# Optimization experiments

Hardware: AMD Instinct MI355X
Metric: run time of the kernel (lower is better)

Reference implementation:

```python
import jax, jax.numpy as jnp
import numpy as np

N_GRID = 16      # reservoir_n
CHANNELS = 4
R = 2            # receptive-field radius -> 5x5 kernel
T_STEPS = 8
NEG_SLOPE = 0.1


def _extract_patches(S):
    # S: [b, C, n, n] -> patches [b, C, 5, 5, n, n] (kernel offsets u,v)
    Sp = jnp.pad(S, ((0, 0), (0, 0), (R, R), (R, R)))
    k = 2 * R + 1
    rows = [jnp.stack([Sp[:, :, du:du + N_GRID, dv:dv + N_GRID] for dv in range(k)], axis=2)
            for du in range(k)]
    return jnp.stack(rows, axis=2)  # [b, C, k, k, n, n]


def _reservoir_step(S, W):
    # W: [n, n, C_out, C_in, k, k]; per-pixel unique weights (locally connected)
    patches = _extract_patches(S)                       # [b, c, u, v, y, x]
    out = jnp.einsum('bcuvyx,yxocuv->boyx', patches, W)  # [b, C, n, n]
    return jnp.where(out > 0, out, NEG_SLOPE * out)      # leaky_relu(0.1)


def setup_inputs() -> dict:
    key = jax.random.key(0)
    k1, k2 = jax.random.split(key)
    x = jax.random.normal(k1, (8192, 784), dtype=jnp.float32)
    # scale weights down so the T-step recurrence stays numerically tame
    W = jax.random.normal(k2, (N_GRID, N_GRID, CHANNELS, CHANNELS, 2 * R + 1, 2 * R + 1),
                          dtype=jnp.float32) * 0.05
    return {"x": x, "W": W}


def reference(x, W):
    batch = x.shape[0]
    total = N_GRID * N_GRID * CHANNELS  # 1024
    padded = jnp.pad(x, ((0, 0), (0, total - x.shape[1])))
    S = padded.reshape(batch, CHANNELS, N_GRID, N_GRID)
    for _ in range(T_STEPS):
        S = _reservoir_step(S, W)
    S_pooled = S.mean(axis=1)                 # pool over channels -> [b, n, n]
    return S_pooled.reshape(batch, -1)        # [b, n*n]
```

## Files before the change

kernel.cpp:

```cpp
#include <hip/hip_runtime.h>

#define NG 16
#define NC 4
#define BPB 16
#define TSTEPS 8
#define PITCH 64
#define CROW (NG * PITCH)

__device__ __forceinline__ void fma4(float w, const float4& s, float4& a) {
    a.x = fmaf(w, s.x, a.x);
    a.y = fmaf(w, s.y, a.y);
    a.z = fmaf(w, s.z, a.z);
    a.w = fmaf(w, s.w, a.w);
}

__device__ __forceinline__ float4 lrelu4(float4 v) {
    float4 r;
    r.x = fmaxf(v.x, 0.1f * v.x);
    r.y = fmaxf(v.y, 0.1f * v.y);
    r.z = fmaxf(v.z, 0.1f * v.z);
    r.w = fmaxf(v.w, 0.1f * v.w);
    return r;
}

template<int CTRL>
__device__ __forceinline__ float dppf(float x) {
    return __int_as_float(__builtin_amdgcn_update_dpp(
        0, __float_as_int(x), CTRL, 0xF, 0xF, true));
}
template<int CTRL>
__device__ __forceinline__ float4 dpp4(float4 v) {
    float4 r;
    r.x = dppf<CTRL>(v.x);
    r.y = dppf<CTRL>(v.y);
    r.z = dppf<CTRL>(v.z);
    r.w = dppf<CTRL>(v.w);
    return r;
}

__global__ void wt_transpose(const float* __restrict__ W, float4* __restrict__ Wt) {
    int t = blockIdx.x * 256 + threadIdx.x;
    if (t >= 25600) return;
    int r = t >> 8;
    int pix = t & 255;
    int c = r / 25, uv = r - c * 25, u = uv / 5, v = uv - u * 5;
    int y = pix >> 4, x = pix & 15;
    float4 w = make_float4(0.f, 0.f, 0.f, 0.f);
    if ((unsigned)(y + u - 2) < 16u && (unsigned)(x + v - 2) < 16u) {
        int base = pix * 400 + c * 25 + uv;
        w.x = W[base];
        w.y = W[base + 100];
        w.z = W[base + 200];
        w.w = W[base + 300];
    }
    Wt[r * 256 + pix] = w;
}

__global__ __launch_bounds__(512, 2)
void reservoir_kernel(const float* __restrict__ X, const float4* __restrict__ Wt,
                      float* __restrict__ out, int batch) {
    __shared__ float4 smv[NC * CROW];
    float* smf = reinterpret_cast<float*>(smv);

    const int tid = threadIdx.x;
    const int oct = tid >> 8;
    const int pix = tid & 255;
    const int y = pix >> 4;
    const int x = pix & 15;
    const long itemBase = (long)blockIdx.x * BPB;

    const int sw = (x >> 1) & 3;
    const int xb = x << 2;
    const int q0 = (2 * oct) ^ sw;
    const int q1 = (2 * oct + 1) ^ sw;

    for (int b = 0; b < BPB; ++b) {
        long item = itemBase + b;
        #pragma unroll
        for (int k = 0; k < 2; ++k) {
            int idx = tid + k * 512;
            float v = 0.f;
            if (idx < 784 && item < batch)
                v = __builtin_nontemporal_load(&X[item * 784 + idx]);
            int c = idx >> 8, rem = idx & 255, yy = rem >> 4, xx = rem & 15;
            int phys = (b >> 2) ^ ((xx >> 1) & 3);
            smf[(((c * NG + yy) << 6) + (xx << 2) + phys) * 4 + (b & 3)] = v;
        }
    }

    const float4* Wp = Wt + pix;
    float4 w0 = Wp[0], w1 = Wp[256], w2 = Wp[512], w3 = Wp[768], w4 = Wp[1024];
    int wnext = 1280;

    __syncthreads();

#define TAP(WV, T0, T1) \
    fma4(WV.x, T0, a00); fma4(WV.x, T1, a01); \
    fma4(WV.y, T0, a10); fma4(WV.y, T1, a11); \
    fma4(WV.z, T0, a20); fma4(WV.z, T1, a21); \
    fma4(WV.w, T0, a30); fma4(WV.w, T1, a31);

    #pragma unroll 1
    for (int t = 0; t < TSTEPS; ++t) {
        float4 a00 = {0,0,0,0}, a01 = {0,0,0,0};
        float4 a10 = {0,0,0,0}, a11 = {0,0,0,0};
        float4 a20 = {0,0,0,0}, a21 = {0,0,0,0};
        float4 a30 = {0,0,0,0}, a31 = {0,0,0,0};

        #pragma unroll 1
        for (int c = 0; c < NC; ++c) {
            #pragma unroll 1
            for (int u = 0; u < 5; ++u) {
                int yy = y + u - 2;
                yy = yy < 0 ? 0 : (yy > 15 ? 15 : yy);
                const int rb = ((c * NG + yy) << 6) + xb;
                const float4 s0 = smv[rb + q0];
                const float4 s1 = smv[rb + q1];

                TAP(w2, s0, s1)
                w2 = Wp[wnext + 512];
                { const float4 t0 = dpp4<0x111>(s0), t1 = dpp4<0x111>(s1);
                  TAP(w1, t0, t1) }
                w1 = Wp[wnext + 256];
                { const float4 t0 = dpp4<0x101>(s0), t1 = dpp4<0x101>(s1);
                  TAP(w3, t0, t1) }
                w3 = Wp[wnext + 768];
                { const float4 t0 = dpp4<0x112>(s0), t1 = dpp4<0x112>(s1);
                  TAP(w0, t0, t1) }
                w0 = Wp[wnext];
                { const float4 t0 = dpp4<0x102>(s0), t1 = dpp4<0x102>(s1);
                  TAP(w4, t0, t1) }
                w4 = Wp[wnext + 1024];

                wnext += 1280;
                if (wnext >= 25600) wnext = 0;
            }
        }

        a00 = lrelu4(a00); a01 = lrelu4(a01);
        a10 = lrelu4(a10); a11 = lrelu4(a11);
        a20 = lrelu4(a20); a21 = lrelu4(a21);
        a30 = lrelu4(a30); a31 = lrelu4(a31);

        if (t < TSTEPS - 1) {
            __syncthreads();
            const int pb = (y << 6) + xb;
            smv[0 * CROW + pb + q0] = a00;  smv[0 * CROW + pb + q1] = a01;
            smv[1 * CROW + pb + q0] = a10;  smv[1 * CROW + pb + q1] = a11;
            smv[2 * CROW + pb + q0] = a20;  smv[2 * CROW + pb + q1] = a21;
            smv[3 * CROW + pb + q0] = a30;  smv[3 * CROW + pb + q1] = a31;
            __syncthreads();
        } else {
            float4 p0, p1;
            p0.x = (a00.x + a10.x + a20.x + a30.x) * 0.25f;
            p0.y = (a00.y + a10.y + a20.y + a30.y) * 0.25f;
            p0.z = (a00.z + a10.z + a20.z + a30.z) * 0.25f;
            p0.w = (a00.w + a10.w + a20.w + a30.w) * 0.25f;
            p1.x = (a01.x + a11.x + a21.x + a31.x) * 0.25f;
            p1.y = (a01.y + a11.y + a21.y + a31.y) * 0.25f;
            p1.z = (a01.z + a11.z + a21.z + a31.z) * 0.25f;
            p1.w = (a01.w + a11.w + a21.w + a31.w) * 0.25f;
            const long b0 = itemBase + 8 * oct;
            const long ob = b0 * 256 + pix;
            if (b0 + 0 < batch) __builtin_nontemporal_store(p0.x, &out[ob + 0 * 256]);
            if (b0 + 1 < batch) __builtin_nontemporal_store(p0.y, &out[ob + 1 * 256]);
            if (b0 + 2 < batch) __builtin_nontemporal_store(p0.z, &out[ob + 2 * 256]);
            if (b0 + 3 < batch) __builtin_nontemporal_store(p0.w, &out[ob + 3 * 256]);
            if (b0 + 4 < batch) __builtin_nontemporal_store(p1.x, &out[ob + 4 * 256]);
            if (b0 + 5 < batch) __builtin_nontemporal_store(p1.y, &out[ob + 5 * 256]);
            if (b0 + 6 < batch) __builtin_nontemporal_store(p1.z, &out[ob + 6 * 256]);
            if (b0 + 7 < batch) __builtin_nontemporal_store(p1.w, &out[ob + 7 * 256]);
        }
    }
}

extern "C" void kernel_launch(void* const* d_in, const int* in_sizes, int n_in,
                              void* d_out, int out_size, void* d_ws, size_t ws_size,
                              hipStream_t stream) {
    const float* X = (const float*)d_in[0];
    const float* W = (const float*)d_in[1];
    float* out = (float*)d_out;
    const int batch = in_sizes[0] / 784;
    const int blocks = (batch + BPB - 1) / BPB;

    wt_transpose<<<100, 256, 0, stream>>>(W, (float4*)d_ws);
    reservoir_kernel<<<blocks, 512, 0, stream>>>(
        X, (const float4*)d_ws, out, batch);
}
```

Measured before the change: 233.3 us.

## Halve block to 8 items and double-buffer state to drop one barrier per step

Each block now handles 8 batch items with 256 threads instead of 16 items with 512 threads. The reservoir state in shared memory is ping-ponged between two buffers, so the barrier before the write-back can be removed and only one __syncthreads per step remains. The shared-memory layout and swizzle are reworked for the new pitch. In exchange there are twice as many blocks, each loading the weight stream from global/L2 again, which doubles weight traffic per item, and the new swizzle may bring bank conflicts.

```diff
diff --git a/kernel.cpp b/kernel.cpp
--- a/kernel.cpp
+++ b/kernel.cpp
@@ -2,10 +2,8 @@
 
 #define NG 16
 #define NC 4
-#define BPB 16
+#define BPB 8
 #define TSTEPS 8
-#define PITCH 64
-#define CROW (NG * PITCH)
 
 __device__ __forceinline__ void fma4(float w, const float4& s, float4& a) {
     a.x = fmaf(w, s.x, a.x);
@@ -56,39 +54,36 @@
     Wt[r * 256 + pix] = w;
 }
 
-__global__ __launch_bounds__(512, 2)
+__global__ __launch_bounds__(256, 2)
 void reservoir_kernel(const float* __restrict__ X, const float4* __restrict__ Wt,
                       float* __restrict__ out, int batch) {
-    __shared__ float4 smv[NC * CROW];
+    __shared__ float4 smv[2 * NC * NG * NG * 2];
     float* smf = reinterpret_cast<float*>(smv);
 
     const int tid = threadIdx.x;
-    const int oct = tid >> 8;
-    const int pix = tid & 255;
-    const int y = pix >> 4;
-    const int x = pix & 15;
+    const int y = tid >> 4;
+    const int x = tid & 15;
     const long itemBase = (long)blockIdx.x * BPB;
 
-    const int sw = (x >> 1) & 3;
-    const int xb = x << 2;
-    const int q0 = (2 * oct) ^ sw;
-    const int q1 = (2 * oct + 1) ^ sw;
+    const int swx = (x >> 2) & 1;
+    const int q0 = swx;
+    const int q1 = swx ^ 1;
 
     for (int b = 0; b < BPB; ++b) {
         long item = itemBase + b;
         #pragma unroll
-        for (int k = 0; k < 2; ++k) {
-            int idx = tid + k * 512;
+        for (int k = 0; k < 4; ++k) {
+            int idx = tid + k * 256;
             float v = 0.f;
             if (idx < 784 && item < batch)
                 v = __builtin_nontemporal_load(&X[item * 784 + idx]);
             int c = idx >> 8, rem = idx & 255, yy = rem >> 4, xx = rem & 15;
-            int phys = (b >> 2) ^ ((xx >> 1) & 3);
-            smf[(((c * NG + yy) << 6) + (xx << 2) + phys) * 4 + (b & 3)] = v;
+            int phys = (b >> 2) ^ ((xx >> 2) & 1);
+            smf[((((c * NG + yy) * NG + xx) << 1) + phys) * 4 + (b & 3)] = v;
         }
     }
 
-    const float4* Wp = Wt + pix;
+    const float4* Wp = Wt + tid;
     float4 w0 = Wp[0], w1 = Wp[256], w2 = Wp[512], w3 = Wp[768], w4 = Wp[1024];
     int wnext = 1280;
 
@@ -102,6 +97,8 @@
 
     #pragma unroll 1
     for (int t = 0; t < TSTEPS; ++t) {
+        const int rbase = (t & 1) << 11;
+        const int wbase = rbase ^ 2048;
         float4 a00 = {0,0,0,0}, a01 = {0,0,0,0};
         float4 a10 = {0,0,0,0}, a11 = {0,0,0,0};
         float4 a20 = {0,0,0,0}, a21 = {0,0,0,0};
@@ -113,7 +110,7 @@
             for (int u = 0; u < 5; ++u) {
                 int yy = y + u - 2;
                 yy = yy < 0 ? 0 : (yy > 15 ? 15 : yy);
-                const int rb = ((c * NG + yy) << 6) + xb;
+                const int rb = rbase + (((c * NG + yy) * NG + x) << 1);
                 const float4 s0 = smv[rb + q0];
                 const float4 s1 = smv[rb + q1];
 
@@ -143,12 +140,11 @@
         a30 = lrelu4(a30); a31 = lrelu4(a31);
 
         if (t < TSTEPS - 1) {
-            __syncthreads();
-            const int pb = (y << 6) + xb;
-            smv[0 * CROW + pb + q0] = a00;  smv[0 * CROW + pb + q1] = a01;
-            smv[1 * CROW + pb + q0] = a10;  smv[1 * CROW + pb + q1] = a11;
-            smv[2 * CROW + pb + q0] = a20;  smv[2 * CROW + pb + q1] = a21;
-            smv[3 * CROW + pb + q0] = a30;  smv[3 * CROW + pb + q1] = a31;
+            const int pb = wbase + (((y * NG) + x) << 1);
+            smv[pb + 0 * 512 + q0] = a00;  smv[pb + 0 * 512 + q1] = a01;
+            smv[pb + 1 * 512 + q0] = a10;  smv[pb + 1 * 512 + q1] = a11;
+            smv[pb + 2 * 512 + q0] = a20;  smv[pb + 2 * 512 + q1] = a21;
+            smv[pb + 3 * 512 + q0] = a30;  smv[pb + 3 * 512 + q1] = a31;
             __syncthreads();
         } else {
             float4 p0, p1;
@@ -160,16 +156,15 @@
             p1.y = (a01.y + a11.y + a21.y + a31.y) * 0.25f;
             p1.z = (a01.z + a11.z + a21.z + a31.z) * 0.25f;
             p1.w = (a01.w + a11.w + a21.w + a31.w) * 0.25f;
-            const long b0 = itemBase + 8 * oct;
-            const long ob = b0 * 256 + pix;
-            if (b0 + 0 < batch) __builtin_nontemporal_store(p0.x, &out[ob + 0 * 256]);
-            if (b0 + 1 < batch) __builtin_nontemporal_store(p0.y, &out[ob + 1 * 256]);
-            if (b0 + 2 < batch) __builtin_nontemporal_store(p0.z, &out[ob + 2 * 256]);
-            if (b0 + 3 < batch) __builtin_nontemporal_store(p0.w, &out[ob + 3 * 256]);
-            if (b0 + 4 < batch) __builtin_nontemporal_store(p1.x, &out[ob + 4 * 256]);
-            if (b0 + 5 < batch) __builtin_nontemporal_store(p1.y, &out[ob + 5 * 256]);
-            if (b0 + 6 < batch) __builtin_nontemporal_store(p1.z, &out[ob + 6 * 256]);
-            if (b0 + 7 < batch) __builtin_nontemporal_store(p1.w, &out[ob + 7 * 256]);
+            const long ob = itemBase * 256 + tid;
+            if (itemBase + 0 < batch) __builtin_nontemporal_store(p0.x, &out[ob + 0 * 256]);
+            if (itemBase + 1 < batch) __builtin_nontemporal_store(p0.y, &out[ob + 1 * 256]);
+            if (itemBase + 2 < batch) __builtin_nontemporal_store(p0.z, &out[ob + 2 * 256]);
+            if (itemBase + 3 < batch) __builtin_nontemporal_store(p0.w, &out[ob + 3 * 256]);
+            if (itemBase + 4 < batch) __builtin_nontemporal_store(p1.x, &out[ob + 4 * 256]);
+            if (itemBase + 5 < batch) __builtin_nontemporal_store(p1.y, &out[ob + 5 * 256]);
+            if (itemBase + 6 < batch) __builtin_nontemporal_store(p1.z, &out[ob + 6 * 256]);
+            if (itemBase + 7 < batch) __builtin_nontemporal_store(p1.w, &out[ob + 7 * 256]);
         }
     }
 }
@@ -184,6 +179,6 @@
     const int blocks = (batch + BPB - 1) / BPB;
 
     wt_transpose<<<100, 256, 0, stream>>>(W, (float4*)d_ws);
-    reservoir_kernel<<<blocks, 512, 0, stream>>>(
+    reservoir_kernel<<<blocks, 256, 0, stream>>>(
         X, (const float4*)d_ws, out, batch);
 }
```

After: 236.6 us. Within noise of the previous version (+1.4%).
